# Performance work log

Measured on AMD Instinct MI355X. Metric: run time of the kernel, lower is better.

## Reference

```python
import jax, jax.numpy as jnp
import numpy as np

N_HEAD = 16

def setup_inputs() -> dict:
    key = jax.random.key(0)
    ks = jax.random.split(key, 5)
    B, T, C = 2, 2048, 1024
    s = 0.02
    return {
        "x": jax.random.normal(ks[0], (B, T, C), jnp.float32),
        "W_attn": jax.random.normal(ks[1], (3 * C, C), jnp.float32) * s,
        "b_attn": jax.random.normal(ks[2], (3 * C,), jnp.float32) * s,
        "W_proj": jax.random.normal(ks[3], (C, C), jnp.float32) * s,
        "b_proj": jax.random.normal(ks[4], (C,), jnp.float32) * s,
    }

def reference(x, W_attn, b_attn, W_proj, b_proj):
    B, T, C = x.shape
    H = N_HEAD
    D = C // H
    # fused QKV projection (torch Linear: y = x @ W.T + b)
    qkv = jnp.einsum('btc,fc->btf', x, W_attn) + b_attn  # [B,T,3C]
    q, k, v = jnp.split(qkv, 3, axis=-1)
    def to_heads(t):
        return t.reshape(B, T, H, D).transpose(0, 2, 1, 3)  # [B,H,T,D]
    q, k, v = to_heads(q), to_heads(k), to_heads(v)
    scale = 1.0 / jnp.sqrt(jnp.array(D, x.dtype))
    scores = jnp.einsum('bhqd,bhkd->bhqk', q, k) * scale  # [B,H,T,T]
    causal = jnp.tril(jnp.ones((T, T), bool))
    scores = jnp.where(causal, scores, jnp.finfo(x.dtype).min)
    p = jax.nn.softmax(scores, axis=-1)
    y = jnp.einsum('bhqk,bhkd->bhqd', p, v)  # [B,H,T,D]
    y = y.transpose(0, 2, 1, 3).reshape(B, T, C)
    out = jnp.einsum('btc,oc->bto', y, W_proj) + b_proj
    return out
```

## Files before the change

### kernel.cpp

```cpp
#include <hip/hip_runtime.h>

typedef unsigned int u32;
typedef unsigned short u16;
typedef __attribute__((ext_vector_type(8))) short bf16x8;
typedef __attribute__((ext_vector_type(4))) float f32x4;

#define T_ 2048
#define HEADS 16
#define DH 64
#define NQ (2 * HEADS * T_ * DH)

__device__ __forceinline__ u16 f2bf(float f) {
    union { float f; u32 u; } x; x.f = f;
    return (u16)((x.u + 0x7fffu + ((x.u >> 16) & 1u)) >> 16);
}
__device__ __forceinline__ u32 pkbf(float lo, float hi) {
    u32 r;
    asm("v_cvt_pk_bf16_f32 %0, %1, %2" : "=v"(r) : "v"(lo), "v"(hi));
    return r;
}
__device__ __forceinline__ void gll16(const void* g, void* l) {
    __builtin_amdgcn_global_load_lds(
        (const __attribute__((address_space(1))) void*)g,
        (__attribute__((address_space(3))) void*)l, 16, 0, 0);
}

#define QSCALE 0.18033688011112042f
#define DEFER_THR 8.0f

#define NG_X  (4096 * 128)
#define NG_WA (3072 * 128)
__global__ __launch_bounds__(256) void cvt_all(
    const float* __restrict__ x, const float* __restrict__ wa,
    const float* __restrict__ wp,
    u16* __restrict__ dx, u16* __restrict__ dwa, u16* __restrict__ dwp)
{
    int gid = blockIdx.x * 256 + threadIdx.x;
    const float* src; u16* dst;
    if (gid < NG_X)                { src = x;  dst = dx; }
    else if (gid < NG_X + NG_WA)   { src = wa; dst = dwa; gid -= NG_X; }
    else                           { src = wp; dst = dwp; gid -= NG_X + NG_WA; }
    const int m = gid >> 7, s = gid & 127;
    const int kt = s >> 3, seg = s & 7;
    const float4 a0 = *(const float4*)&src[m * 1024 + s * 8];
    const float4 a1 = *(const float4*)&src[m * 1024 + s * 8 + 4];
    uint4 t;
    t.x = pkbf(a0.x, a0.y); t.y = pkbf(a0.z, a0.w);
    t.z = pkbf(a1.x, a1.y); t.w = pkbf(a1.z, a1.w);
    const int mt = m >> 7, r = m & 127;
    char* d = (char*)dst + ((size_t)(mt * 16 + kt)) * 16384
              + r * 128 + ((seg ^ (r & 7)) << 4);
    *(uint4*)d = t;
}

template<int EPI>
__global__ __launch_bounds__(256, 3) void gemm_lds(
    const char* __restrict__ At, const char* __restrict__ Bt,
    const float* __restrict__ bias,
    u16* __restrict__ q, u16* __restrict__ k, u16* __restrict__ vt,
    float* __restrict__ outF)
{
    __shared__ __align__(16) char AsB[16384];
    __shared__ __align__(16) char BsB[16384];
    const int tid = threadIdx.x;
    const int l = tid & 63, li = l & 15, lg = l >> 4;
    const int w = tid >> 6, wm = w >> 1, wn = w & 1;
    const int m0 = blockIdx.y * 128, n0 = blockIdx.x * 128;
    const char* Ab = At + (size_t)blockIdx.y * (16 * 16384);
    const char* Bb = Bt + (size_t)blockIdx.x * (16 * 16384);

    f32x4 acc[4][4];
    #pragma unroll
    for (int i = 0; i < 4; ++i)
        #pragma unroll
        for (int j = 0; j < 4; ++j) acc[i][j] = (f32x4){0.f, 0.f, 0.f, 0.f};

    for (int kt = 0; kt < 16; ++kt) {
        const char* An = Ab + kt * 16384;
        const char* Bn = Bb + kt * 16384;
        #pragma unroll
        for (int i = 0; i < 4; ++i) {
            gll16(An + w * 4096 + i * 1024 + l * 16, &AsB[w * 4096 + i * 1024]);
            gll16(Bn + w * 4096 + i * 1024 + l * 16, &BsB[w * 4096 + i * 1024]);
        }
        asm volatile("s_waitcnt vmcnt(0)" ::: "memory");
        __syncthreads();
        #pragma unroll
        for (int kc = 0; kc < 2; ++kc) {
            const int key = ((kc * 4 + lg) ^ (li & 7)) << 4;
            bf16x8 a[4], b[4];
            #pragma unroll
            for (int f = 0; f < 4; ++f)
                a[f] = *(const bf16x8*)&AsB[(wm * 64 + f * 16 + li) * 128 + key];
            #pragma unroll
            for (int f = 0; f < 4; ++f)
                b[f] = *(const bf16x8*)&BsB[(wn * 64 + f * 16 + li) * 128 + key];
            #pragma unroll
            for (int mi = 0; mi < 4; ++mi)
                #pragma unroll
                for (int ni = 0; ni < 4; ++ni)
                    acc[mi][ni] = __builtin_amdgcn_mfma_f32_16x16x32_bf16(a[mi], b[ni], acc[mi][ni], 0, 0, 0);
        }
        __syncthreads();
    }

    const int mb = m0 + wm * 64;
    const int nb0 = n0 + wn * 64;
    if constexpr (EPI == 0) {
        const int part = n0 >> 10;
        if (part < 2) {
            u16* dst = (part == 0) ? q : k;
            const float scl = (part == 0) ? QSCALE : 1.0f;
            #pragma unroll
            for (int mi = 0; mi < 4; ++mi)
                #pragma unroll
                for (int r = 0; r < 4; ++r) {
                    const int m = mb + mi * 16 + lg * 4 + r;
                    const int bb = m >> 11, t = m & 2047;
                    #pragma unroll
                    for (int ni = 0; ni < 4; ++ni) {
                        const int n = nb0 + ni * 16 + li;
                        const int c = n & 1023;
                        const int h = c >> 6, d = c & 63;
                        const float val = (acc[mi][ni][r] + bias[n]) * scl;
                        dst[(((bb << 4) + h) * T_ + t) * DH + d] = f2bf(val);
                    }
                }
        } else {
            #pragma unroll
            for (int mi = 0; mi < 4; ++mi) {
                const int m = mb + mi * 16 + lg * 4;
                const int bb = m >> 11, t0 = m & 2047;
                #pragma unroll
                for (int ni = 0; ni < 4; ++ni) {
                    const int n = nb0 + ni * 16 + li;
                    const int c = n & 1023;
                    const int h = c >> 6, d = c & 63;
                    const float bz = bias[n];
                    u32 w0 = pkbf(acc[mi][ni][0] + bz, acc[mi][ni][1] + bz);
                    u32 w1 = pkbf(acc[mi][ni][2] + bz, acc[mi][ni][3] + bz);
                    *(uint2*)&vt[(((bb << 4) + h) * 64 + d) * (size_t)T_ + t0] = make_uint2(w0, w1);
                }
            }
        }
    } else {
        #pragma unroll
        for (int mi = 0; mi < 4; ++mi)
            #pragma unroll
            for (int r = 0; r < 4; ++r) {
                const int m = mb + mi * 16 + lg * 4 + r;
                #pragma unroll
                for (int ni = 0; ni < 4; ++ni) {
                    const int n = nb0 + ni * 16 + li;
                    outF[m * 1024 + n] = acc[mi][ni][r] + bias[n];
                }
            }
    }
}

__global__ __launch_bounds__(256, 2) void flash_attn(
    const u16* __restrict__ Q, const u16* __restrict__ K,
    const u16* __restrict__ Vt, char* __restrict__ Yt)
{
    __shared__ __align__(16) char KsB[2][8192];
    __shared__ __align__(16) char VsB[2][8192];
    __shared__ __align__(16) char PsB[4][2048];

    const int bh = blockIdx.x;
    const int slot = blockIdx.y;
    const int qt = (slot & 1) ? (31 - (slot >> 1)) : (slot >> 1);
    const int tid = threadIdx.x;
    const int w  = tid >> 6;
    const int l  = tid & 63;
    const int li = l & 15, lg = l >> 4;
    const u16* Qb = Q  + (size_t)bh * (T_ * DH);
    const u16* Kb = K  + (size_t)bh * (T_ * DH);
    const u16* Vb = Vt + (size_t)bh * (T_ * DH);
    const int srow = tid >> 3;
    const int sseg = tid & 7;
    char* Pw = PsB[w];
    const int b = bh >> 4, h = bh & 15;
    const int skey = (srow & 7) << 4;
    const int rdkey = (li & 7) << 4;

    const int wq0 = qt * 64 + w * 16;
    const int q_row = wq0 + li;
    const int nkv = qt + 1;

    bf16x8 qa[2];
    qa[0] = *(const bf16x8*)(Qb + q_row * 64 + 0  + lg * 8);
    qa[1] = *(const bf16x8*)(Qb + q_row * 64 + 32 + lg * 8);

    f32x4 o[4];
    #pragma unroll
    for (int nb = 0; nb < 4; ++nb) o[nb] = (f32x4){0.f, 0.f, 0.f, 0.f};
    float m_r = -INFINITY, l_r = 0.f;

    uint4 kr0, kr1, vr0, vr1;
    kr0 = *(const uint4*)(Kb + srow * 64 + sseg * 8);
    kr1 = *(const uint4*)(Kb + (srow + 32) * 64 + sseg * 8);
    vr0 = *(const uint4*)(Vb + (size_t)srow * T_ + sseg * 8);
    vr1 = *(const uint4*)(Vb + (size_t)(srow + 32) * T_ + sseg * 8);
    *(uint4*)&KsB[0][srow * 128        + ((sseg << 4) ^ skey)] = kr0;
    *(uint4*)&KsB[0][(srow + 32) * 128 + ((sseg << 4) ^ skey)] = kr1;
    *(uint4*)&VsB[0][srow * 128        + ((sseg << 4) ^ skey)] = vr0;
    *(uint4*)&VsB[0][(srow + 32) * 128 + ((sseg << 4) ^ skey)] = vr1;
    __syncthreads();

    for (int j = 0; j < nkv; ++j) {
        const int cur = j & 1;
        const bool has_next = (j + 1 < nkv);
        if (has_next) {
            const int t0 = (j + 1) * 64;
            kr0 = *(const uint4*)(Kb + (t0 + srow) * 64 + sseg * 8);
            kr1 = *(const uint4*)(Kb + (t0 + srow + 32) * 64 + sseg * 8);
            vr0 = *(const uint4*)(Vb + (size_t)srow * T_ + t0 + sseg * 8);
            vr1 = *(const uint4*)(Vb + (size_t)(srow + 32) * T_ + t0 + sseg * 8);
        }
        const char* Kc = KsB[cur];
        f32x4 s[4];
        __builtin_amdgcn_s_setprio(1);
        #pragma unroll
        for (int f = 0; f < 4; ++f) {
            s[f] = (f32x4){0.f, 0.f, 0.f, 0.f};
            #pragma unroll
            for (int c = 0; c < 2; ++c) {
                bf16x8 kb = *(const bf16x8*)&Kc[(f * 16 + li) * 128 + ((c * 64 + lg * 16) ^ rdkey)];
                s[f] = __builtin_amdgcn_mfma_f32_16x16x32_bf16(kb, qa[c], s[f], 0, 0, 0);
            }
        }
        __builtin_amdgcn_s_setprio(0);
        if ((j + 1) * 64 > wq0) {
            const int kbase = j * 64 + lg * 4;
            #pragma unroll
            for (int f = 0; f < 4; ++f)
                #pragma unroll
                for (int r = 0; r < 4; ++r)
                    if (kbase + f * 16 + r > q_row) s[f][r] = -INFINITY;
        }
        float lm = s[0][0];
        #pragma unroll
        for (int f = 0; f < 4; ++f)
            #pragma unroll
            for (int r = 0; r < 4; ++r) lm = fmaxf(lm, s[f][r]);
        if (!__all(lm <= m_r + DEFER_THR)) {
            float tm = lm;
            tm = fmaxf(tm, __shfl_xor(tm, 16));
            tm = fmaxf(tm, __shfl_xor(tm, 32));
            const float mnew = fmaxf(m_r, tm);
            const float corr = exp2f(m_r - mnew);
            m_r = mnew;
            l_r *= corr;
            #pragma unroll
            for (int nb = 0; nb < 4; ++nb)
                #pragma unroll
                for (int r = 0; r < 4; ++r) o[nb][r] *= corr;
        }
        #pragma unroll
        for (int f = 0; f < 4; ++f) {
            float p0 = exp2f(s[f][0] - m_r);
            float p1 = exp2f(s[f][1] - m_r);
            float p2 = exp2f(s[f][2] - m_r);
            float p3 = exp2f(s[f][3] - m_r);
            l_r += (p0 + p1) + (p2 + p3);
            uint2 pk = make_uint2(pkbf(p0, p1), pkbf(p2, p3));
            *(uint2*)&Pw[li * 128 + (((f * 32 + lg * 8)) ^ rdkey)] = pk;
        }
        if (has_next) {
            *(uint4*)&KsB[cur ^ 1][srow * 128        + ((sseg << 4) ^ skey)] = kr0;
            *(uint4*)&KsB[cur ^ 1][(srow + 32) * 128 + ((sseg << 4) ^ skey)] = kr1;
            *(uint4*)&VsB[cur ^ 1][srow * 128        + ((sseg << 4) ^ skey)] = vr0;
            *(uint4*)&VsB[cur ^ 1][(srow + 32) * 128 + ((sseg << 4) ^ skey)] = vr1;
        }
        const char* Vc = VsB[cur];
        __builtin_amdgcn_s_setprio(1);
        #pragma unroll
        for (int c = 0; c < 2; ++c) {
            bf16x8 pa = *(const bf16x8*)&Pw[li * 128 + ((c * 64 + lg * 16) ^ rdkey)];
            #pragma unroll
            for (int nb = 0; nb < 4; ++nb) {
                bf16x8 vb = *(const bf16x8*)&Vc[(nb * 16 + li) * 128 + ((c * 64 + lg * 16) ^ rdkey)];
                o[nb] = __builtin_amdgcn_mfma_f32_16x16x32_bf16(vb, pa, o[nb], 0, 0, 0);
            }
        }
        __builtin_amdgcn_s_setprio(0);
        __syncthreads();
    }

    l_r += __shfl_xor(l_r, 16);
    l_r += __shfl_xor(l_r, 32);
    const float inv = 1.0f / l_r;
    const int r128 = (qt & 1) * 64 + w * 16 + li;
    const int rk = (r128 & 7) << 4;
    char* yrow = Yt + ((size_t)((b * 16 + (qt >> 1)) * 16 + h)) * 16384 + r128 * 128;
    #pragma unroll
    for (int nb = 0; nb < 4; ++nb) {
        const int seg = 2 * nb + (lg >> 1);
        uint2 pk = make_uint2(pkbf(o[nb][0] * inv, o[nb][1] * inv),
                              pkbf(o[nb][2] * inv, o[nb][3] * inv));
        *(uint2*)&yrow[((seg << 4) ^ rk) + (lg & 1) * 8] = pk;
    }
}

extern "C" void kernel_launch(void* const* d_in, const int* in_sizes, int n_in,
                              void* d_out, int out_size, void* d_ws, size_t ws_size,
                              hipStream_t stream) {
    const float* x      = (const float*)d_in[0];
    const float* W_attn = (const float*)d_in[1];
    const float* b_attn = (const float*)d_in[2];
    const float* W_proj = (const float*)d_in[3];
    const float* b_proj = (const float*)d_in[4];
    float* out = (float*)d_out;

    char* ws = (char*)d_ws;
    u16* q   = (u16*)ws;
    u16* k   = (u16*)(ws + (8u << 20));
    u16* vt  = (u16*)(ws + (16u << 20));
    char* xb = ws + (24u << 20);
    char* wab = ws + (32u << 20);
    char* wpb = ws + (38u << 20);

    cvt_all<<<4096, 256, 0, stream>>>(x, W_attn, W_proj, (u16*)xb, (u16*)wab, (u16*)wpb);
    gemm_lds<0><<<dim3(24, 32), 256, 0, stream>>>(xb, wab, b_attn, q, k, vt, nullptr);
    flash_attn<<<dim3(32, 32), 256, 0, stream>>>(q, k, vt, xb );
    gemm_lds<1><<<dim3(8, 32), 256, 0, stream>>>(xb , wpb, b_proj,
                                                 nullptr, nullptr, nullptr, out);
}
```

Measured before the change: 109.5 us.

## Pair causal query tiles per block and switch attention to 32x32 MFMA

Each flash-attention block now handles two query tiles (px and 31-px), split across its four waves, so the causal work per block is balanced and the grid halves. K/V tiles loaded into LDS are shared by both query tiles, which cuts global loads. The QK and PV products move from 16x16x32 to 32x32x16 MFMA, with 32 query rows per wave, and the LDS swizzle keys and P buffer layout change to match. The cost is that waves on the shorter tile sit idle in later iterations while still joining the barriers, and each wave holds more accumulator registers.

```diff
diff --git a/kernel.cpp b/kernel.cpp
--- a/kernel.cpp
+++ b/kernel.cpp
@@ -4,11 +4,11 @@
 typedef unsigned short u16;
 typedef __attribute__((ext_vector_type(8))) short bf16x8;
 typedef __attribute__((ext_vector_type(4))) float f32x4;
+typedef __attribute__((ext_vector_type(16))) float f32x16;
 
 #define T_ 2048
 #define HEADS 16
 #define DH 64
-#define NQ (2 * HEADS * T_ * DH)
 
 __device__ __forceinline__ u16 f2bf(float f) {
     union { float f; u32 u; } x; x.f = f;
@@ -164,36 +164,43 @@
 {
     __shared__ __align__(16) char KsB[2][8192];
     __shared__ __align__(16) char VsB[2][8192];
-    __shared__ __align__(16) char PsB[4][2048];
+    __shared__ __align__(16) char PsB[4][4096];
 
     const int bh = blockIdx.x;
-    const int slot = blockIdx.y;
-    const int qt = (slot & 1) ? (31 - (slot >> 1)) : (slot >> 1);
+    const int px = blockIdx.y;
     const int tid = threadIdx.x;
     const int w  = tid >> 6;
     const int l  = tid & 63;
-    const int li = l & 15, lg = l >> 4;
+    const int q5 = l & 31, hi = l >> 5;
     const u16* Qb = Q  + (size_t)bh * (T_ * DH);
     const u16* Kb = K  + (size_t)bh * (T_ * DH);
     const u16* Vb = Vt + (size_t)bh * (T_ * DH);
+    char* Pw = PsB[w];
+    const int b = bh >> 4, h = bh & 15;
+
+    const int myqt = (w < 2) ? px : (31 - px);
+    const int wq0 = myqt * 64 + (w & 1) * 32;
+    const int q_row = wq0 + q5;
+    const int nb = 32 - px;
+
     const int srow = tid >> 3;
     const int sseg = tid & 7;
-    char* Pw = PsB[w];
-    const int b = bh >> 4, h = bh & 15;
-    const int skey = (srow & 7) << 4;
-    const int rdkey = (li & 7) << 4;
-
-    const int wq0 = qt * 64 + w * 16;
-    const int q_row = wq0 + li;
-    const int nkv = qt + 1;
-
-    bf16x8 qa[2];
-    qa[0] = *(const bf16x8*)(Qb + q_row * 64 + 0  + lg * 8);
-    qa[1] = *(const bf16x8*)(Qb + q_row * 64 + 32 + lg * 8);
-
-    f32x4 o[4];
+    const int skey0 = ((srow ^ (srow >> 3)) & 7) << 4;
+    const int skey1 = ((srow ^ ((srow >> 3) + 4)) & 7) << 4;
+    const int keyA0 = ((q5 ^ (q5 >> 3)) & 7) << 4;
+    const int keyA1 = ((q5 ^ ((q5 >> 3) + 4)) & 7) << 4;
+    const int pkey  = keyA0;
+
+    bf16x8 qa[4];
     #pragma unroll
-    for (int nb = 0; nb < 4; ++nb) o[nb] = (f32x4){0.f, 0.f, 0.f, 0.f};
+    for (int kd = 0; kd < 4; ++kd)
+        qa[kd] = *(const bf16x8*)(Qb + q_row * 64 + kd * 16 + hi * 8);
+
+    f32x16 o2[2];
+    #pragma unroll
+    for (int mf = 0; mf < 2; ++mf)
+        #pragma unroll
+        for (int r = 0; r < 16; ++r) o2[mf][r] = 0.f;
     float m_r = -INFINITY, l_r = 0.f;
 
     uint4 kr0, kr1, vr0, vr1;
@@ -201,15 +208,16 @@
     kr1 = *(const uint4*)(Kb + (srow + 32) * 64 + sseg * 8);
     vr0 = *(const uint4*)(Vb + (size_t)srow * T_ + sseg * 8);
     vr1 = *(const uint4*)(Vb + (size_t)(srow + 32) * T_ + sseg * 8);
-    *(uint4*)&KsB[0][srow * 128        + ((sseg << 4) ^ skey)] = kr0;
-    *(uint4*)&KsB[0][(srow + 32) * 128 + ((sseg << 4) ^ skey)] = kr1;
-    *(uint4*)&VsB[0][srow * 128        + ((sseg << 4) ^ skey)] = vr0;
-    *(uint4*)&VsB[0][(srow + 32) * 128 + ((sseg << 4) ^ skey)] = vr1;
+    *(uint4*)&KsB[0][srow * 128        + ((sseg << 4) ^ skey0)] = kr0;
+    *(uint4*)&KsB[0][(srow + 32) * 128 + ((sseg << 4) ^ skey1)] = kr1;
+    *(uint4*)&VsB[0][srow * 128        + ((sseg << 4) ^ skey0)] = vr0;
+    *(uint4*)&VsB[0][(srow + 32) * 128 + ((sseg << 4) ^ skey1)] = vr1;
     __syncthreads();
 
-    for (int j = 0; j < nkv; ++j) {
+    for (int j = 0; j < nb; ++j) {
         const int cur = j & 1;
-        const bool has_next = (j + 1 < nkv);
+        const bool has_next = (j + 1 < nb);
+        const bool act = (j <= myqt);
         if (has_next) {
             const int t0 = (j + 1) * 64;
             kr0 = *(const uint4*)(Kb + (t0 + srow) * 64 + sseg * 8);
@@ -217,89 +225,101 @@
             vr0 = *(const uint4*)(Vb + (size_t)srow * T_ + t0 + sseg * 8);
             vr1 = *(const uint4*)(Vb + (size_t)(srow + 32) * T_ + t0 + sseg * 8);
         }
-        const char* Kc = KsB[cur];
-        f32x4 s[4];
-        __builtin_amdgcn_s_setprio(1);
-        #pragma unroll
-        for (int f = 0; f < 4; ++f) {
-            s[f] = (f32x4){0.f, 0.f, 0.f, 0.f};
-            #pragma unroll
-            for (int c = 0; c < 2; ++c) {
-                bf16x8 kb = *(const bf16x8*)&Kc[(f * 16 + li) * 128 + ((c * 64 + lg * 16) ^ rdkey)];
-                s[f] = __builtin_amdgcn_mfma_f32_16x16x32_bf16(kb, qa[c], s[f], 0, 0, 0);
-            }
-        }
-        __builtin_amdgcn_s_setprio(0);
-        if ((j + 1) * 64 > wq0) {
-            const int kbase = j * 64 + lg * 4;
-            #pragma unroll
-            for (int f = 0; f < 4; ++f)
-                #pragma unroll
-                for (int r = 0; r < 4; ++r)
-                    if (kbase + f * 16 + r > q_row) s[f][r] = -INFINITY;
-        }
-        float lm = s[0][0];
-        #pragma unroll
-        for (int f = 0; f < 4; ++f)
-            #pragma unroll
-            for (int r = 0; r < 4; ++r) lm = fmaxf(lm, s[f][r]);
-        if (!__all(lm <= m_r + DEFER_THR)) {
-            float tm = lm;
-            tm = fmaxf(tm, __shfl_xor(tm, 16));
-            tm = fmaxf(tm, __shfl_xor(tm, 32));
-            const float mnew = fmaxf(m_r, tm);
-            const float corr = exp2f(m_r - mnew);
-            m_r = mnew;
-            l_r *= corr;
-            #pragma unroll
-            for (int nb = 0; nb < 4; ++nb)
-                #pragma unroll
-                for (int r = 0; r < 4; ++r) o[nb][r] *= corr;
-        }
-        #pragma unroll
-        for (int f = 0; f < 4; ++f) {
-            float p0 = exp2f(s[f][0] - m_r);
-            float p1 = exp2f(s[f][1] - m_r);
-            float p2 = exp2f(s[f][2] - m_r);
-            float p3 = exp2f(s[f][3] - m_r);
-            l_r += (p0 + p1) + (p2 + p3);
-            uint2 pk = make_uint2(pkbf(p0, p1), pkbf(p2, p3));
-            *(uint2*)&Pw[li * 128 + (((f * 32 + lg * 8)) ^ rdkey)] = pk;
+        f32x16 s2[2];
+        if (act) {
+            const char* Kc = KsB[cur];
+            __builtin_amdgcn_s_setprio(1);
+            #pragma unroll
+            for (int mf = 0; mf < 2; ++mf) {
+                #pragma unroll
+                for (int r = 0; r < 16; ++r) s2[mf][r] = 0.f;
+                const int rbase = (mf ? 32 : 0) + q5;
+                const int ka = mf ? keyA1 : keyA0;
+                #pragma unroll
+                for (int kd = 0; kd < 4; ++kd) {
+                    bf16x8 kb = *(const bf16x8*)&Kc[rbase * 128 + ((((2 * kd + hi) << 4)) ^ ka)];
+                    s2[mf] = __builtin_amdgcn_mfma_f32_32x32x16_bf16(kb, qa[kd], s2[mf], 0, 0, 0);
+                }
+            }
+            __builtin_amdgcn_s_setprio(0);
+            if ((j + 1) * 64 > wq0) {
+                const int kb0 = j * 64 + hi * 4;
+                #pragma unroll
+                for (int mf = 0; mf < 2; ++mf)
+                    #pragma unroll
+                    for (int r = 0; r < 16; ++r) {
+                        const int kk = kb0 + (mf ? 32 : 0) + (r & 3) + ((r & 12) << 1);
+                        if (kk > q_row) s2[mf][r] = -INFINITY;
+                    }
+            }
+            float lm = s2[0][0];
+            #pragma unroll
+            for (int mf = 0; mf < 2; ++mf)
+                #pragma unroll
+                for (int r = 0; r < 16; ++r) lm = fmaxf(lm, s2[mf][r]);
+            const float tm = fmaxf(lm, __shfl_xor(lm, 32));
+            if (!__all(tm <= m_r + DEFER_THR)) {
+                const float mnew = fmaxf(m_r, tm);
+                const float corr = exp2f(m_r - mnew);
+                m_r = mnew;
+                l_r *= corr;
+                #pragma unroll
+                for (int mf = 0; mf < 2; ++mf)
+                    #pragma unroll
+                    for (int r = 0; r < 16; ++r) o2[mf][r] *= corr;
+            }
+            #pragma unroll
+            for (int mf = 0; mf < 2; ++mf)
+                #pragma unroll
+                for (int m = 0; m < 4; ++m) {
+                    const float p0 = exp2f(s2[mf][4 * m + 0] - m_r);
+                    const float p1 = exp2f(s2[mf][4 * m + 1] - m_r);
+                    const float p2 = exp2f(s2[mf][4 * m + 2] - m_r);
+                    const float p3 = exp2f(s2[mf][4 * m + 3] - m_r);
+                    l_r += (p0 + p1) + (p2 + p3);
+                    uint2 pk = make_uint2(pkbf(p0, p1), pkbf(p2, p3));
+                    *(uint2*)&Pw[q5 * 128 + ((((mf ? 4 : 0) + m) << 4) ^ pkey) + 8 * hi] = pk;
+                }
         }
         if (has_next) {
-            *(uint4*)&KsB[cur ^ 1][srow * 128        + ((sseg << 4) ^ skey)] = kr0;
-            *(uint4*)&KsB[cur ^ 1][(srow + 32) * 128 + ((sseg << 4) ^ skey)] = kr1;
-            *(uint4*)&VsB[cur ^ 1][srow * 128        + ((sseg << 4) ^ skey)] = vr0;
-            *(uint4*)&VsB[cur ^ 1][(srow + 32) * 128 + ((sseg << 4) ^ skey)] = vr1;
-        }
-        const char* Vc = VsB[cur];
-        __builtin_amdgcn_s_setprio(1);
-        #pragma unroll
-        for (int c = 0; c < 2; ++c) {
-            bf16x8 pa = *(const bf16x8*)&Pw[li * 128 + ((c * 64 + lg * 16) ^ rdkey)];
-            #pragma unroll
-            for (int nb = 0; nb < 4; ++nb) {
-                bf16x8 vb = *(const bf16x8*)&Vc[(nb * 16 + li) * 128 + ((c * 64 + lg * 16) ^ rdkey)];
-                o[nb] = __builtin_amdgcn_mfma_f32_16x16x32_bf16(vb, pa, o[nb], 0, 0, 0);
-            }
-        }
-        __builtin_amdgcn_s_setprio(0);
+            *(uint4*)&KsB[cur ^ 1][srow * 128        + ((sseg << 4) ^ skey0)] = kr0;
+            *(uint4*)&KsB[cur ^ 1][(srow + 32) * 128 + ((sseg << 4) ^ skey1)] = kr1;
+            *(uint4*)&VsB[cur ^ 1][srow * 128        + ((sseg << 4) ^ skey0)] = vr0;
+            *(uint4*)&VsB[cur ^ 1][(srow + 32) * 128 + ((sseg << 4) ^ skey1)] = vr1;
+        }
+        if (act) {
+            const char* Vc = VsB[cur];
+            __builtin_amdgcn_s_setprio(1);
+            #pragma unroll
+            for (int ks = 0; ks < 4; ++ks) {
+                bf16x8 pb = *(const bf16x8*)&Pw[q5 * 128 + (((2 * ks + hi) << 4) ^ pkey)];
+                #pragma unroll
+                for (int mf = 0; mf < 2; ++mf) {
+                    const int rbase = (mf ? 32 : 0) + q5;
+                    const int ka = mf ? keyA1 : keyA0;
+                    bf16x8 va = *(const bf16x8*)&Vc[rbase * 128 + (((2 * ks + hi) << 4) ^ ka)];
+                    o2[mf] = __builtin_amdgcn_mfma_f32_32x32x16_bf16(va, pb, o2[mf], 0, 0, 0);
+                }
+            }
+            __builtin_amdgcn_s_setprio(0);
+        }
         __syncthreads();
     }
 
-    l_r += __shfl_xor(l_r, 16);
     l_r += __shfl_xor(l_r, 32);
     const float inv = 1.0f / l_r;
-    const int r128 = (qt & 1) * 64 + w * 16 + li;
+    const int r128 = (myqt & 1) * 64 + (w & 1) * 32 + q5;
     const int rk = (r128 & 7) << 4;
-    char* yrow = Yt + ((size_t)((b * 16 + (qt >> 1)) * 16 + h)) * 16384 + r128 * 128;
+    char* yrow = Yt + ((size_t)((b * 16 + (myqt >> 1)) * 16 + h)) * 16384 + r128 * 128;
     #pragma unroll
-    for (int nb = 0; nb < 4; ++nb) {
-        const int seg = 2 * nb + (lg >> 1);
-        uint2 pk = make_uint2(pkbf(o[nb][0] * inv, o[nb][1] * inv),
-                              pkbf(o[nb][2] * inv, o[nb][3] * inv));
-        *(uint2*)&yrow[((seg << 4) ^ rk) + (lg & 1) * 8] = pk;
-    }
+    for (int mf = 0; mf < 2; ++mf)
+        #pragma unroll
+        for (int m = 0; m < 4; ++m) {
+            uint2 pk = make_uint2(
+                pkbf(o2[mf][4 * m + 0] * inv, o2[mf][4 * m + 1] * inv),
+                pkbf(o2[mf][4 * m + 2] * inv, o2[mf][4 * m + 3] * inv));
+            *(uint2*)&yrow[((((mf ? 4 : 0) + m) << 4) ^ rk) + 8 * hi] = pk;
+        }
 }
 
 extern "C" void kernel_launch(void* const* d_in, const int* in_sizes, int n_in,
@@ -322,7 +342,7 @@
 
     cvt_all<<<4096, 256, 0, stream>>>(x, W_attn, W_proj, (u16*)xb, (u16*)wab, (u16*)wpb);
     gemm_lds<0><<<dim3(24, 32), 256, 0, stream>>>(xb, wab, b_attn, q, k, vt, nullptr);
-    flash_attn<<<dim3(32, 32), 256, 0, stream>>>(q, k, vt, xb );
+    flash_attn<<<dim3(32, 16), 256, 0, stream>>>(q, k, vt, xb );
     gemm_lds<1><<<dim3(8, 32), 256, 0, stream>>>(xb , wpb, b_proj,
                                                  nullptr, nullptr, nullptr, out);
 }
```

Result: slower. 121.5 us (+11.0%).
